# Kernel tuning notes

Hardware: AMD Instinct MI355X
Metric: run time of the kernel (lower is better)

The kernel has to match this reference:

```python
import jax, jax.numpy as jnp
import numpy as np

HEADS = 8
D_MODEL = 512
D_K = D_MODEL // HEADS


def setup_inputs() -> dict:
    key = jax.random.key(0)
    ks = jax.random.split(key, 12)
    B, S = 2, 4096
    scale = 1.0 / np.sqrt(D_MODEL)
    inp = {
        "q": jax.random.normal(ks[0], (B, S, D_MODEL), jnp.float32),
        "k": jax.random.normal(ks[1], (B, S, D_MODEL), jnp.float32),
        "v": jax.random.normal(ks[2], (B, S, D_MODEL), jnp.float32),
        "mask": jax.random.randint(ks[3], (B, 1, 1, S), 0, 2, jnp.int32),
        "wq": jax.random.normal(ks[4], (D_MODEL, D_MODEL), jnp.float32) * scale,
        "bq": jnp.zeros((D_MODEL,), jnp.float32),
        "wk": jax.random.normal(ks[5], (D_MODEL, D_MODEL), jnp.float32) * scale,
        "bk": jnp.zeros((D_MODEL,), jnp.float32),
        "wv": jax.random.normal(ks[6], (D_MODEL, D_MODEL), jnp.float32) * scale,
        "bv": jnp.zeros((D_MODEL,), jnp.float32),
        "wo": jax.random.normal(ks[7], (D_MODEL, D_MODEL), jnp.float32) * scale,
        "bo": jnp.zeros((D_MODEL,), jnp.float32),
    }
    return inp


def reference(q, k, v, mask, wq, bq, wk, bk, wv, bv, wo, bo):
    B, S, _ = q.shape
    # torch nn.Linear: y = x @ W.T + b
    qh = (q @ wq.T + bq).reshape(B, S, HEADS, D_K).transpose(0, 2, 1, 3)  # b h s d
    kh = (k @ wk.T + bk).reshape(B, S, HEADS, D_K).transpose(0, 2, 1, 3)
    vh = (v @ wv.T + bv).reshape(B, S, HEADS, D_K).transpose(0, 2, 1, 3)
    scores = jnp.einsum("bhqd,bhkd->bhqk", qh, kh) / jnp.sqrt(jnp.float32(D_K))
    scores = jnp.where(mask == 0, jnp.float32(-1e9), scores)
    attn = jax.nn.softmax(scores, axis=-1)  # dropout is identity in eval mode
    out = jnp.einsum("bhqk,bhkd->bhqd", attn, vh)
    out = out.transpose(0, 2, 1, 3).reshape(B, S, D_MODEL)
    return out @ wo.T + bo
```

## Files before the change

kernel.cpp:

```cpp
#include <hip/hip_runtime.h>
#include <hip/hip_bf16.h>

#define S 4096
#define DM 512
#define HH 8
#define DK 64
#define MT 8192

typedef __attribute__((ext_vector_type(8)))  short bf16x8;
typedef __attribute__((ext_vector_type(4)))  float f32x4;
typedef __attribute__((ext_vector_type(16))) float f32x16;
typedef __attribute__((ext_vector_type(4)))  unsigned int u32x4;

#define CQ 0.18033688011112042f

__device__ __forceinline__ short f2bs(float x) {
    __hip_bfloat16 h = __float2bfloat16(x);
    return *reinterpret_cast<short*>(&h);
}

__device__ __forceinline__ bf16x8 pack8(const float4& a, const float4& b) {
    bf16x8 r;
    r[0] = f2bs(a.x); r[1] = f2bs(a.y); r[2] = f2bs(a.z); r[3] = f2bs(a.w);
    r[4] = f2bs(b.x); r[5] = f2bs(b.y); r[6] = f2bs(b.z); r[7] = f2bs(b.w);
    return r;
}

__device__ __forceinline__ unsigned cvtpk(float lo, float hi) {
    unsigned r;
    asm("v_cvt_pk_bf16_f32 %0, %1, %2" : "=v"(r) : "v"(lo), "v"(hi));
    return r;
}

__device__ __forceinline__ bf16x8 mk_pb(unsigned a, unsigned b, unsigned c, unsigned d) {
    u32x4 t; t[0] = a; t[1] = b; t[2] = c; t[3] = d;
    return __builtin_bit_cast(bf16x8, t);
}

__device__ __forceinline__ void gld_lds16(const void* gp, void* lp) {
    __builtin_amdgcn_global_load_lds(
        (const __attribute__((address_space(1))) void*)gp,
        (__attribute__((address_space(3))) void*)lp, 16, 0, 0);
}
__device__ __forceinline__ void gld_lds4(const void* gp, void* lp) {
    __builtin_amdgcn_global_load_lds(
        (const __attribute__((address_space(1))) void*)gp,
        (__attribute__((address_space(3))) void*)lp, 4, 0, 0);
}

__global__ __launch_bounds__(256, 4)
void qkv_gemm(const float* __restrict__ Xq, const float* __restrict__ Xk,
              const float* __restrict__ Xv,
              const float* __restrict__ Wq, const float* __restrict__ Wk,
              const float* __restrict__ Wv,
              const float* __restrict__ Bq, const float* __restrict__ Bk,
              const float* __restrict__ Bv,
              const int* __restrict__ mask, float* __restrict__ maskf,
              unsigned short* __restrict__ Yq, unsigned short* __restrict__ Yk,
              unsigned short* __restrict__ Yv)
{
    __shared__ char As[128 * 128];
    __shared__ char Bs[64 * 128];
    const int bid  = blockIdx.x;
    const int t = threadIdx.x;
    if (bid < 32) {
        int i = bid * 256 + t;
        maskf[i] = mask[i] ? 0.f : -3e38f;
    }
    const int work = (bid & 7) * 192 + (bid >> 3);
    const int gp   = work >> 3;
    const int mat  = gp >> 6;
    const int m0   = (gp & 63) * 128;
    const int n0   = (work & 7) * 64;
    const float* X    = mat == 0 ? Xq : (mat == 1 ? Xk : Xv);
    const float* W    = mat == 0 ? Wq : (mat == 1 ? Wk : Wv);
    const float* bias = mat == 0 ? Bq : (mat == 1 ? Bk : Bv);

    const int l = t & 63, w = t >> 6;
    const int wr = w >> 1, wc = w & 1;
    const int lr = l & 15, lg = l >> 4;
    const int srow = t >> 3, schk = t & 7;
    const int sswz = (schk ^ (srow & 7)) * 16;

    float4 fA[4][2]; float4 fB[2][2];
    auto loadA = [&](int k0) {
        #pragma unroll
        for (int i = 0; i < 4; ++i) {
            const float* p = X + (size_t)(m0 + srow + 32 * i) * DM + k0 + schk * 8;
            fA[i][0] = *(const float4*)p;
            fA[i][1] = *(const float4*)(p + 4);
        }
    };
    auto loadB = [&](int k0) {
        #pragma unroll
        for (int i = 0; i < 2; ++i) {
            const float* p = W + (size_t)(n0 + srow + 32 * i) * DM + k0 + schk * 8;
            fB[i][0] = *(const float4*)p;
            fB[i][1] = *(const float4*)(p + 4);
        }
    };

    loadA(0); loadB(0);

    f32x4 acc[4][2];
    #pragma unroll
    for (int fm = 0; fm < 4; ++fm)
        #pragma unroll
        for (int fn = 0; fn < 2; ++fn) acc[fm][fn] = f32x4{0.f, 0.f, 0.f, 0.f};

    #pragma unroll
    for (int kt = 0; kt < 8; ++kt) {
        bf16x8 wA[4], wB[2];
        #pragma unroll
        for (int i = 0; i < 4; ++i) wA[i] = pack8(fA[i][0], fA[i][1]);
        #pragma unroll
        for (int i = 0; i < 2; ++i) wB[i] = pack8(fB[i][0], fB[i][1]);

        if (kt < 7) { loadA((kt + 1) * 64); loadB((kt + 1) * 64); }

        __syncthreads();
        #pragma unroll
        for (int i = 0; i < 4; ++i)
            *(bf16x8*)(As + (srow + 32 * i) * 128 + sswz) = wA[i];
        #pragma unroll
        for (int i = 0; i < 2; ++i)
            *(bf16x8*)(Bs + (srow + 32 * i) * 128 + sswz) = wB[i];
        __syncthreads();

        #pragma unroll
        for (int kc = 0; kc < 2; ++kc) {
            bf16x8 af[4], bfr[2];
            #pragma unroll
            for (int fm = 0; fm < 4; ++fm) {
                int row = wr * 64 + fm * 16 + lr;
                af[fm] = *(const bf16x8*)(As + row * 128 + (((kc * 4 + lg) ^ (row & 7)) * 16));
            }
            #pragma unroll
            for (int fn = 0; fn < 2; ++fn) {
                int row = wc * 32 + fn * 16 + lr;
                bfr[fn] = *(const bf16x8*)(Bs + row * 128 + (((kc * 4 + lg) ^ (row & 7)) * 16));
            }
            #pragma unroll
            for (int fm = 0; fm < 4; ++fm)
                #pragma unroll
                for (int fn = 0; fn < 2; ++fn)
                    acc[fm][fn] = __builtin_amdgcn_mfma_f32_16x16x32_bf16(af[fm], bfr[fn], acc[fm][fn], 0, 0, 0);
        }
    }

    #pragma unroll
    for (int fm = 0; fm < 4; ++fm) {
        #pragma unroll
        for (int fn = 0; fn < 2; ++fn) {
            int n = n0 + wc * 32 + fn * 16 + lr;
            float bn = bias[n];
            int mbase = m0 + wr * 64 + fm * 16 + lg * 4;
            int h = n >> 6, d = n & 63;
            int bb = mbase >> 12, s0 = mbase & (S - 1);
            if (mat == 0) {
                #pragma unroll
                for (int r = 0; r < 4; ++r)
                    Yq[(((size_t)(bb * HH + h)) * S + s0 + r) * DK + d] =
                        (unsigned short)f2bs((acc[fm][fn][r] + bn) * CQ);
            } else if (mat == 1) {
                int c   = (d >> 4) & 3;
                int hi2 = (d >> 3) & 1;
                int ii  = d & 7;
                size_t blkb = ((((size_t)(bb * HH + h)) * 128 + (s0 >> 5)) * 4 + c) * 512;
                int lanebase = (s0 & 31) + 32 * hi2;
                #pragma unroll
                for (int r = 0; r < 4; ++r)
                    Yk[blkb + (size_t)(lanebase + r) * 8 + ii] =
                        (unsigned short)f2bs(acc[fm][fn][r] + bn);
            } else {
                int dt2  = (d >> 5) & 1;
                int hi_s = (s0 >> 3) & 1;
                int lane = (d & 31) + 32 * hi_s;
                size_t base = ((((size_t)(bb * HH + h)) * 256 + (s0 >> 4)) * 2 + dt2) * 512
                            + (size_t)lane * 8 + (s0 & 7);
                ushort4 u;
                u.x = (unsigned short)f2bs(acc[fm][fn][0] + bn);
                u.y = (unsigned short)f2bs(acc[fm][fn][1] + bn);
                u.z = (unsigned short)f2bs(acc[fm][fn][2] + bn);
                u.w = (unsigned short)f2bs(acc[fm][fn][3] + bn);
                *(ushort4*)(Yv + base) = u;
            }
        }
    }
}

__global__ __launch_bounds__(256, 2)
void out_gemm(const short* __restrict__ Xb, const float* __restrict__ W,
              const float* __restrict__ bias, float* __restrict__ Y)
{
    __shared__ char As[128 * 128];
    __shared__ char Bs[64 * 128];
    const int bid  = blockIdx.x;
    const int work = (bid & 7) * 64 + (bid >> 3);
    const int n0 = (work & 7) * 64;
    const int m0 = (work >> 3) * 128;

    const int t = threadIdx.x, l = t & 63, w = t >> 6;
    const int wr = w >> 1, wc = w & 1;
    const int lr = l & 15, lg = l >> 4;
    const int srow = t >> 3, schk = t & 7;
    const int sswz = (schk ^ (srow & 7)) * 16;

    float4 fB[2][2]; bf16x8 rA[4];
    auto loadA = [&](int k0) {
        #pragma unroll
        for (int i = 0; i < 4; ++i)
            rA[i] = *(const bf16x8*)(Xb + (size_t)(m0 + srow + 32 * i) * DM + k0 + schk * 8);
    };
    auto loadB = [&](int k0) {
        #pragma unroll
        for (int i = 0; i < 2; ++i) {
            const float* p = W + (size_t)(n0 + srow + 32 * i) * DM + k0 + schk * 8;
            fB[i][0] = *(const float4*)p;
            fB[i][1] = *(const float4*)(p + 4);
        }
    };

    loadA(0); loadB(0);

    f32x4 acc[4][2];
    #pragma unroll
    for (int fm = 0; fm < 4; ++fm)
        #pragma unroll
        for (int fn = 0; fn < 2; ++fn) acc[fm][fn] = f32x4{0.f, 0.f, 0.f, 0.f};

    #pragma unroll
    for (int kt = 0; kt < 8; ++kt) {
        bf16x8 wA[4], wB[2];
        #pragma unroll
        for (int i = 0; i < 4; ++i) wA[i] = rA[i];
        #pragma unroll
        for (int i = 0; i < 2; ++i) wB[i] = pack8(fB[i][0], fB[i][1]);

        if (kt < 7) { loadA((kt + 1) * 64); loadB((kt + 1) * 64); }

        __syncthreads();
        #pragma unroll
        for (int i = 0; i < 4; ++i)
            *(bf16x8*)(As + (srow + 32 * i) * 128 + sswz) = wA[i];
        #pragma unroll
        for (int i = 0; i < 2; ++i)
            *(bf16x8*)(Bs + (srow + 32 * i) * 128 + sswz) = wB[i];
        __syncthreads();

        #pragma unroll
        for (int kc = 0; kc < 2; ++kc) {
            bf16x8 af[4], bfr[2];
            #pragma unroll
            for (int fm = 0; fm < 4; ++fm) {
                int row = wr * 64 + fm * 16 + lr;
                af[fm] = *(const bf16x8*)(As + row * 128 + (((kc * 4 + lg) ^ (row & 7)) * 16));
            }
            #pragma unroll
            for (int fn = 0; fn < 2; ++fn) {
                int row = wc * 32 + fn * 16 + lr;
                bfr[fn] = *(const bf16x8*)(Bs + row * 128 + (((kc * 4 + lg) ^ (row & 7)) * 16));
            }
            #pragma unroll
            for (int fm = 0; fm < 4; ++fm)
                #pragma unroll
                for (int fn = 0; fn < 2; ++fn)
                    acc[fm][fn] = __builtin_amdgcn_mfma_f32_16x16x32_bf16(af[fm], bfr[fn], acc[fm][fn], 0, 0, 0);
        }
    }

    #pragma unroll
    for (int fm = 0; fm < 4; ++fm) {
        #pragma unroll
        for (int fn = 0; fn < 2; ++fn) {
            int n = n0 + wc * 32 + fn * 16 + lr;
            float bn = bias[n];
            int mbase = m0 + wr * 64 + fm * 16 + lg * 4;
            #pragma unroll
            for (int r = 0; r < 4; ++r)
                Y[(size_t)(mbase + r) * DM + n] = acc[fm][fn][r] + bn;
        }
    }
}

__global__ __launch_bounds__(256, 4)
void flash_mfma(const short* __restrict__ qh,
                const short* __restrict__ kfb,
                const short* __restrict__ vfb,
                const float* __restrict__ maskf,
                unsigned short* __restrict__ att)
{
    const int bid  = blockIdx.x;
    const int work = (bid & 7) * 128 + (bid >> 3);
    const int bh = work >> 6, b = bh >> 3, h = bh & 7;
    const int q0 = (work & 63) * 64;
    const int t = threadIdx.x, w = t >> 6, l = t & 63;
    const int l31 = l & 31, hi = l >> 5;
    const int kw = w & 1, qw = w >> 1;

    __shared__ char sBuf[2 * 16384 + 2 * 256];
    char*  B0 = sBuf;
    char*  B1 = sBuf + 16384;
    float* M0 = (float*)(sBuf + 32768);
    float* M1 = (float*)(sBuf + 32768 + 256);

    const short* qg = qh + ((size_t)bh * S + q0 + qw * 32 + l31) * DK;
    bf16x8 qf[4];
    #pragma unroll
    for (int c = 0; c < 4; ++c)
        qf[c] = *(const bf16x8*)(qg + c * 16 + hi * 8);

    f32x16 oc[2];
    #pragma unroll
    for (int dt = 0; dt < 2; ++dt)
        #pragma unroll
        for (int r = 0; r < 16; ++r) oc[dt][r] = 0.f;
    float ls = 0.f;

    const char* kg0 = (const char*)(kfb + (size_t)bh * 262144) + (size_t)l * 16;
    const char* vg0 = (const char*)(vfb + (size_t)bh * 262144) + (size_t)l * 16;
    const char* mg0 = (const char*)(maskf + b * S) + (size_t)l * 4;

    auto stage = [&](char* dst, float* mdst, int step) {
        const char* kg = kg0 + (size_t)step * 8192;
        const char* vg = vg0 + (size_t)step * 8192;
        #pragma unroll
        for (int i = 0; i < 4; ++i) {
            int chunk = w * 4 + i;
            const char* g = (chunk < 8) ? (kg + chunk * 1024) : (vg + (chunk - 8) * 1024);
            gld_lds16(g, dst + chunk * 1024);
        }
        if (w == 0) gld_lds4(mg0 + (size_t)step * 256, mdst);
    };

    auto compute = [&](const char* kv, const float* mlds) {
        const char* mb = (const char*)mlds + kw * 128 + hi * 16;
        f32x4 m40 = *(const f32x4*)(mb);
        f32x4 m41 = *(const f32x4*)(mb + 32);
        f32x4 m42 = *(const f32x4*)(mb + 64);
        f32x4 m43 = *(const f32x4*)(mb + 96);
        f32x16 sc;
        #pragma unroll
        for (int o = 0; o < 4; ++o) {
            sc[o] = m40[o]; sc[4 + o] = m41[o];
            sc[8 + o] = m42[o]; sc[12 + o] = m43[o];
        }
        const char* kbase = kv + kw * 4096 + l * 16;
        bf16x8 kf0 = *(const bf16x8*)(kbase);
        bf16x8 kf1 = *(const bf16x8*)(kbase + 1024);
        bf16x8 kf2 = *(const bf16x8*)(kbase + 2048);
        bf16x8 kf3 = *(const bf16x8*)(kbase + 3072);
        __builtin_amdgcn_s_setprio(1);
        sc = __builtin_amdgcn_mfma_f32_32x32x16_bf16(kf0, qf[0], sc, 0, 0, 0);
        sc = __builtin_amdgcn_mfma_f32_32x32x16_bf16(kf1, qf[1], sc, 0, 0, 0);
        sc = __builtin_amdgcn_mfma_f32_32x32x16_bf16(kf2, qf[2], sc, 0, 0, 0);
        sc = __builtin_amdgcn_mfma_f32_32x32x16_bf16(kf3, qf[3], sc, 0, 0, 0);
        __builtin_amdgcn_s_setprio(0);

        const char* vbase = kv + 8192 + kw * 4096 + l * 16;
        bf16x8 vf00 = *(const bf16x8*)(vbase);
        bf16x8 vf01 = *(const bf16x8*)(vbase + 1024);
        bf16x8 vf10 = *(const bf16x8*)(vbase + 2048);
        bf16x8 vf11 = *(const bf16x8*)(vbase + 3072);

        float p[16];
        #pragma unroll
        for (int r = 0; r < 16; ++r) p[r] = exp2f(sc[r]);
        float a0 = 0.f;
        #pragma unroll
        for (int r = 0; r < 16; r += 4)
            a0 += (p[r] + p[r + 1]) + (p[r + 2] + p[r + 3]);
        ls += a0;

        unsigned A0 = cvtpk(p[0],  p[1]),  B0r = cvtpk(p[2],  p[3]);
        unsigned A1 = cvtpk(p[4],  p[5]),  B1r = cvtpk(p[6],  p[7]);
        unsigned A2 = cvtpk(p[8],  p[9]),  B2r = cvtpk(p[10], p[11]);
        unsigned A3 = cvtpk(p[12], p[13]), B3r = cvtpk(p[14], p[15]);
        asm("v_permlane32_swap_b32 %0, %1" : "+v"(A0), "+v"(A1));
        asm("v_permlane32_swap_b32 %0, %1" : "+v"(B0r), "+v"(B1r));
        asm("v_permlane32_swap_b32 %0, %1" : "+v"(A2), "+v"(A3));
        asm("v_permlane32_swap_b32 %0, %1" : "+v"(B2r), "+v"(B3r));
        bf16x8 pb0 = mk_pb(A0, B0r, A1, B1r);
        bf16x8 pb1 = mk_pb(A2, B2r, A3, B3r);

        __builtin_amdgcn_s_setprio(1);
        oc[0] = __builtin_amdgcn_mfma_f32_32x32x16_bf16(vf00, pb0, oc[0], 0, 0, 0);
        oc[1] = __builtin_amdgcn_mfma_f32_32x32x16_bf16(vf01, pb0, oc[1], 0, 0, 0);
        oc[0] = __builtin_amdgcn_mfma_f32_32x32x16_bf16(vf10, pb1, oc[0], 0, 0, 0);
        oc[1] = __builtin_amdgcn_mfma_f32_32x32x16_bf16(vf11, pb1, oc[1], 0, 0, 0);
        __builtin_amdgcn_s_setprio(0);
    };

    stage(B0, M0, 0);
    __syncthreads();

    const int NT = S / 64;
    for (int it = 0; it < NT / 2; ++it) {
        const int s0 = it * 2;
        stage(B1, M1, s0 + 1);
        compute(B0, M0);
        __syncthreads();
        if (s0 + 2 < NT) stage(B0, M0, s0 + 2);
        compute(B1, M1);
        __syncthreads();
    }

    float* scr = (float*)sBuf;
    float* pp  = scr + (size_t)(qw * 64 + l) * 33;
    if (kw == 1) {
        #pragma unroll
        for (int r = 0; r < 16; ++r) { pp[r] = oc[0][r]; pp[16 + r] = oc[1][r]; }
        pp[32] = ls;
    }
    __syncthreads();
    if (kw == 0) {
        #pragma unroll
        for (int r = 0; r < 16; ++r) { oc[0][r] += pp[r]; oc[1][r] += pp[16 + r]; }
        ls += pp[32];
        ls += __shfl_xor(ls, 32);
        const float linv = 1.0f / ls;
        unsigned short* ap = att + ((size_t)(b * S + q0 + qw * 32 + l31)) * DM + h * DK;
        #pragma unroll
        for (int dt = 0; dt < 2; ++dt)
            #pragma unroll
            for (int g = 0; g < 4; ++g) {
                uint2 u;
                u.x = cvtpk(oc[dt][g * 4 + 0] * linv, oc[dt][g * 4 + 1] * linv);
                u.y = cvtpk(oc[dt][g * 4 + 2] * linv, oc[dt][g * 4 + 3] * linv);
                *(uint2*)(ap + dt * 32 + g * 8 + hi * 4) = u;
            }
    }
}

extern "C" void kernel_launch(void* const* d_in, const int* in_sizes, int n_in,
                              void* d_out, int out_size, void* d_ws, size_t ws_size,
                              hipStream_t stream) {
    const float* q    = (const float*)d_in[0];
    const float* k    = (const float*)d_in[1];
    const float* v    = (const float*)d_in[2];
    const int*   mask = (const int*)  d_in[3];
    const float* wq   = (const float*)d_in[4];
    const float* bq   = (const float*)d_in[5];
    const float* wk   = (const float*)d_in[6];
    const float* bk   = (const float*)d_in[7];
    const float* wv   = (const float*)d_in[8];
    const float* bv   = (const float*)d_in[9];
    const float* wo   = (const float*)d_in[10];
    const float* bo   = (const float*)d_in[11];
    float* out = (float*)d_out;

    char* wsb = (char*)d_ws;
    unsigned short* qh    = (unsigned short*)(wsb);
    unsigned short* kfb   = (unsigned short*)(wsb + (size_t)8  * 1024 * 1024);
    unsigned short* vfb   = (unsigned short*)(wsb + (size_t)16 * 1024 * 1024);
    unsigned short* att   = (unsigned short*)(wsb + (size_t)24 * 1024 * 1024);
    float*          maskf = (float*)         (wsb + (size_t)32 * 1024 * 1024);

    dim3 blk(256);
    qkv_gemm<<<dim3(1536), blk, 0, stream>>>(q, k, v, wq, wk, wv, bq, bk, bv,
                                     mask, maskf, qh, kfb, vfb);

    flash_mfma<<<dim3(1024), blk, 0, stream>>>((const short*)qh, (const short*)kfb,
                                     (const short*)vfb, maskf, att);

    out_gemm<<<dim3(512), blk, 0, stream>>>((const short*)att, wo, bo, out);
}
```

Measured before the change: 162.2 us.

## Double flash attention block size to share K/V tiles across 128 query rows

After: 163.6 us. Within noise of the previous version (+0.9%).

```diff
diff --git a/kernel.cpp b/kernel.cpp
--- a/kernel.cpp
+++ b/kernel.cpp
@@ -41,11 +41,6 @@
     __builtin_amdgcn_global_load_lds(
         (const __attribute__((address_space(1))) void*)gp,
         (__attribute__((address_space(3))) void*)lp, 16, 0, 0);
-}
-__device__ __forceinline__ void gld_lds4(const void* gp, void* lp) {
-    __builtin_amdgcn_global_load_lds(
-        (const __attribute__((address_space(1))) void*)gp,
-        (__attribute__((address_space(3))) void*)lp, 4, 0, 0);
 }
 
 __global__ __launch_bounds__(256, 4)
@@ -283,7 +278,7 @@
     }
 }
 
-__global__ __launch_bounds__(256, 4)
+__global__ __launch_bounds__(512, 4)
 void flash_mfma(const short* __restrict__ qh,
                 const short* __restrict__ kfb,
                 const short* __restrict__ vfb,
@@ -291,18 +286,16 @@
                 unsigned short* __restrict__ att)
 {
     const int bid  = blockIdx.x;
-    const int work = (bid & 7) * 128 + (bid >> 3);
-    const int bh = work >> 6, b = bh >> 3, h = bh & 7;
-    const int q0 = (work & 63) * 64;
+    const int work = (bid & 7) * 64 + (bid >> 3);
+    const int bh = work >> 5, b = bh >> 3, h = bh & 7;
+    const int q0 = (work & 31) * 128;
     const int t = threadIdx.x, w = t >> 6, l = t & 63;
     const int l31 = l & 31, hi = l >> 5;
     const int kw = w & 1, qw = w >> 1;
 
-    __shared__ char sBuf[2 * 16384 + 2 * 256];
-    char*  B0 = sBuf;
-    char*  B1 = sBuf + 16384;
-    float* M0 = (float*)(sBuf + 32768);
-    float* M1 = (float*)(sBuf + 32768 + 256);
+    __shared__ char sBuf[34048];
+    char* B0 = sBuf;
+    char* B1 = sBuf + 16384;
 
     const short* qg = qh + ((size_t)bh * S + q0 + qw * 32 + l31) * DK;
     bf16x8 qf[4];
@@ -319,32 +312,28 @@
 
     const char* kg0 = (const char*)(kfb + (size_t)bh * 262144) + (size_t)l * 16;
     const char* vg0 = (const char*)(vfb + (size_t)bh * 262144) + (size_t)l * 16;
-    const char* mg0 = (const char*)(maskf + b * S) + (size_t)l * 4;
-
-    auto stage = [&](char* dst, float* mdst, int step) {
+    const float* mbase_g = maskf + b * S + kw * 32 + hi * 4;
+
+    auto stage = [&](char* dst, int step) {
         const char* kg = kg0 + (size_t)step * 8192;
         const char* vg = vg0 + (size_t)step * 8192;
         #pragma unroll
-        for (int i = 0; i < 4; ++i) {
-            int chunk = w * 4 + i;
+        for (int i = 0; i < 2; ++i) {
+            int chunk = w * 2 + i;
             const char* g = (chunk < 8) ? (kg + chunk * 1024) : (vg + (chunk - 8) * 1024);
             gld_lds16(g, dst + chunk * 1024);
         }
-        if (w == 0) gld_lds4(mg0 + (size_t)step * 256, mdst);
-    };
-
-    auto compute = [&](const char* kv, const float* mlds) {
-        const char* mb = (const char*)mlds + kw * 128 + hi * 16;
-        f32x4 m40 = *(const f32x4*)(mb);
-        f32x4 m41 = *(const f32x4*)(mb + 32);
-        f32x4 m42 = *(const f32x4*)(mb + 64);
-        f32x4 m43 = *(const f32x4*)(mb + 96);
+    };
+
+    auto compute = [&](const char* kv, int step) {
+        const float* mp = mbase_g + step * 64;
         f32x16 sc;
-        #pragma unroll
-        for (int o = 0; o < 4; ++o) {
-            sc[o] = m40[o]; sc[4 + o] = m41[o];
-            sc[8 + o] = m42[o]; sc[12 + o] = m43[o];
-        }
+        float* scp = (float*)&sc;
+        *(f32x4*)(scp + 0)  = *(const f32x4*)(mp);
+        *(f32x4*)(scp + 4)  = *(const f32x4*)(mp + 8);
+        *(f32x4*)(scp + 8)  = *(const f32x4*)(mp + 16);
+        *(f32x4*)(scp + 12) = *(const f32x4*)(mp + 24);
+
         const char* kbase = kv + kw * 4096 + l * 16;
         bf16x8 kf0 = *(const bf16x8*)(kbase);
         bf16x8 kf1 = *(const bf16x8*)(kbase + 1024);
@@ -391,17 +380,17 @@
         __builtin_amdgcn_s_setprio(0);
     };
 
-    stage(B0, M0, 0);
+    stage(B0, 0);
     __syncthreads();
 
     const int NT = S / 64;
     for (int it = 0; it < NT / 2; ++it) {
         const int s0 = it * 2;
-        stage(B1, M1, s0 + 1);
-        compute(B0, M0);
-        __syncthreads();
-        if (s0 + 2 < NT) stage(B0, M0, s0 + 2);
-        compute(B1, M1);
+        stage(B1, s0 + 1);
+        compute(B0, s0);
+        __syncthreads();
+        if (s0 + 2 < NT) stage(B0, s0 + 2);
+        compute(B1, s0 + 1);
         __syncthreads();
     }
 
@@ -460,7 +449,7 @@
     qkv_gemm<<<dim3(1536), blk, 0, stream>>>(q, k, v, wq, wk, wv, bq, bk, bv,
                                      mask, maskf, qh, kfb, vfb);
 
-    flash_mfma<<<dim3(1024), blk, 0, stream>>>((const short*)qh, (const short*)kfb,
+    flash_mfma<<<dim3(512), dim3(512), 0, stream>>>((const short*)qh, (const short*)kfb,
                                      (const short*)vfb, maskf, att);
 
     out_gemm<<<dim3(512), blk, 0, stream>>>((const short*)att, wo, bo, out);
```

## Give each wave private double-buffered K/V staging and drop per-tile block barriers

Applied to the files above, without the earlier changes.

New measurement: 174.6 us. +7.6%, slower.

```diff
diff --git a/kernel.cpp b/kernel.cpp
--- a/kernel.cpp
+++ b/kernel.cpp
@@ -283,7 +283,7 @@
     }
 }
 
-__global__ __launch_bounds__(256, 4)
+__global__ __launch_bounds__(256, 2)
 void flash_mfma(const short* __restrict__ qh,
                 const short* __restrict__ kfb,
                 const short* __restrict__ vfb,
@@ -298,11 +298,10 @@
     const int l31 = l & 31, hi = l >> 5;
     const int kw = w & 1, qw = w >> 1;
 
-    __shared__ char sBuf[2 * 16384 + 2 * 256];
-    char*  B0 = sBuf;
-    char*  B1 = sBuf + 16384;
-    float* M0 = (float*)(sBuf + 32768);
-    float* M1 = (float*)(sBuf + 32768 + 256);
+    __shared__ char sBuf[4 * 16896];
+    char* wbase = sBuf + w * 16896;
+    char* bufA  = wbase;
+    char* bufB  = wbase + 8448;
 
     const short* qg = qh + ((size_t)bh * S + q0 + qw * 32 + l31) * DK;
     bf16x8 qf[4];
@@ -317,24 +316,22 @@
         for (int r = 0; r < 16; ++r) oc[dt][r] = 0.f;
     float ls = 0.f;
 
-    const char* kg0 = (const char*)(kfb + (size_t)bh * 262144) + (size_t)l * 16;
-    const char* vg0 = (const char*)(vfb + (size_t)bh * 262144) + (size_t)l * 16;
+    const char* kgW = (const char*)(kfb + (size_t)bh * 262144) + kw * 4096 + (size_t)l * 16;
+    const char* vgW = (const char*)(vfb + (size_t)bh * 262144) + kw * 4096 + (size_t)l * 16;
     const char* mg0 = (const char*)(maskf + b * S) + (size_t)l * 4;
 
-    auto stage = [&](char* dst, float* mdst, int step) {
-        const char* kg = kg0 + (size_t)step * 8192;
-        const char* vg = vg0 + (size_t)step * 8192;
-        #pragma unroll
-        for (int i = 0; i < 4; ++i) {
-            int chunk = w * 4 + i;
-            const char* g = (chunk < 8) ? (kg + chunk * 1024) : (vg + (chunk - 8) * 1024);
-            gld_lds16(g, dst + chunk * 1024);
-        }
-        if (w == 0) gld_lds4(mg0 + (size_t)step * 256, mdst);
-    };
-
-    auto compute = [&](const char* kv, const float* mlds) {
-        const char* mb = (const char*)mlds + kw * 128 + hi * 16;
+    auto stageW = [&](char* dst, int step) {
+        const char* kg = kgW + (size_t)step * 8192;
+        const char* vg = vgW + (size_t)step * 8192;
+        #pragma unroll
+        for (int i = 0; i < 4; ++i) gld_lds16(kg + i * 1024, dst + i * 1024);
+        #pragma unroll
+        for (int i = 0; i < 4; ++i) gld_lds16(vg + i * 1024, dst + 4096 + i * 1024);
+        gld_lds4(mg0 + (size_t)step * 256, dst + 8192);
+    };
+
+    auto computeW = [&](const char* buf) {
+        const char* mb = buf + 8192 + kw * 128 + hi * 16;
         f32x4 m40 = *(const f32x4*)(mb);
         f32x4 m41 = *(const f32x4*)(mb + 32);
         f32x4 m42 = *(const f32x4*)(mb + 64);
@@ -345,7 +342,7 @@
             sc[o] = m40[o]; sc[4 + o] = m41[o];
             sc[8 + o] = m42[o]; sc[12 + o] = m43[o];
         }
-        const char* kbase = kv + kw * 4096 + l * 16;
+        const char* kbase = buf + l * 16;
         bf16x8 kf0 = *(const bf16x8*)(kbase);
         bf16x8 kf1 = *(const bf16x8*)(kbase + 1024);
         bf16x8 kf2 = *(const bf16x8*)(kbase + 2048);
@@ -357,7 +354,7 @@
         sc = __builtin_amdgcn_mfma_f32_32x32x16_bf16(kf3, qf[3], sc, 0, 0, 0);
         __builtin_amdgcn_s_setprio(0);
 
-        const char* vbase = kv + 8192 + kw * 4096 + l * 16;
+        const char* vbase = buf + 4096 + l * 16;
         bf16x8 vf00 = *(const bf16x8*)(vbase);
         bf16x8 vf01 = *(const bf16x8*)(vbase + 1024);
         bf16x8 vf10 = *(const bf16x8*)(vbase + 2048);
@@ -391,20 +388,31 @@
         __builtin_amdgcn_s_setprio(0);
     };
 
-    stage(B0, M0, 0);
+    stageW(bufA, 0);
+    stageW(bufB, 1);
+
+    for (int it = 0; it < 32; ++it) {
+        const int s0 = it * 2;
+        asm volatile("s_waitcnt vmcnt(9)" ::: "memory");
+        __builtin_amdgcn_sched_barrier(0);
+        computeW(bufA);
+        asm volatile("s_waitcnt lgkmcnt(0)" ::: "memory");
+        __builtin_amdgcn_sched_barrier(0);
+        if (s0 + 2 < 64) stageW(bufA, s0 + 2);
+
+        if (it < 31) {
+            asm volatile("s_waitcnt vmcnt(9)" ::: "memory");
+        } else {
+            asm volatile("s_waitcnt vmcnt(0)" ::: "memory");
+        }
+        __builtin_amdgcn_sched_barrier(0);
+        computeW(bufB);
+        asm volatile("s_waitcnt lgkmcnt(0)" ::: "memory");
+        __builtin_amdgcn_sched_barrier(0);
+        if (s0 + 3 < 64) stageW(bufB, s0 + 3);
+    }
+
     __syncthreads();
-
-    const int NT = S / 64;
-    for (int it = 0; it < NT / 2; ++it) {
-        const int s0 = it * 2;
-        stage(B1, M1, s0 + 1);
-        compute(B0, M0);
-        __syncthreads();
-        if (s0 + 2 < NT) stage(B0, M0, s0 + 2);
-        compute(B1, M1);
-        __syncthreads();
-    }
-
     float* scr = (float*)sBuf;
     float* pp  = scr + (size_t)(qw * 64 + l) * 33;
     if (kw == 1) {
```
